# Performance work log

Hardware: AMD Instinct MI355X
Metric: run time of the kernel (lower is better)

## Reference

```python
import jax, jax.numpy as jnp
import numpy as np

B, C, H, W, K = 4, 64, 128, 128, 3
K2 = K * K
PAD = (K - 1) // 2  # same padding for 3x3


def setup_inputs() -> dict:
    key = jax.random.key(0)
    ks = jax.random.split(key, 9)
    s = 0.05
    return {
        "x": jax.random.normal(ks[0], (B, C, H, W), jnp.float32),
        "inter": jax.random.normal(ks[1], (B, C, H, W), jnp.float32),
        # offset/mask predictor conv: input cat([x, inter]) -> 3*K2 channels (dy, dx, mask)
        "w_offset": jax.random.normal(ks[2], (3 * K2, 2 * C, K, K), jnp.float32) * s,
        "b_offset": jnp.zeros((3 * K2,), jnp.float32),
        # deformable conv weight (bias=False per DGM init)
        "w_dcn": jax.random.normal(ks[3], (C, C, K, K), jnp.float32) * s,
        # SFT gamma branch: two 1x1 convs (bias=False)
        "w_g1": jax.random.normal(ks[4], (C, C), jnp.float32) * s,
        "w_g2": jax.random.normal(ks[5], (C, C), jnp.float32) * s,
        # SFT beta branch: two 1x1 convs (bias=False)
        "w_b1": jax.random.normal(ks[6], (C, C), jnp.float32) * s,
        "w_b2": jax.random.normal(ks[7], (C, C), jnp.float32) * s,
    }


def _lrelu(v):
    # LeakyReLU(0.1)
    return jnp.where(v >= 0, v, 0.1 * v)


def _conv(x, w, b=None):
    y = jax.lax.conv_general_dilated(
        x, w, window_strides=(1, 1), padding=[(PAD, PAD), (PAD, PAD)],
        dimension_numbers=("NCHW", "OIHW", "NCHW"))
    if b is not None:
        y = y + b[None, :, None, None]
    return y


def _bilinear_gather(x, py, px):
    """x: [B,C,H,W]; py, px: [B,K2,H,W] float sample coords.
    Returns samples [B,K2,H,W,C]; out-of-bounds treated as zero (DCN zero-pad)."""
    y0 = jnp.floor(py)
    x0 = jnp.floor(px)
    wy = (py - y0)[..., None]
    wx = (px - x0)[..., None]

    def gather(yi, xi):
        valid = ((yi >= 0) & (yi < H) & (xi >= 0) & (xi < W)).astype(x.dtype)
        yc = jnp.clip(yi, 0, H - 1).astype(jnp.int32)
        xc = jnp.clip(xi, 0, W - 1).astype(jnp.int32)
        bidx = jnp.arange(B)[:, None, None, None]
        v = x[bidx, :, yc, xc]  # advanced indexing -> [B,K2,H,W,C]
        return v * valid[..., None]

    v00 = gather(y0, x0)
    v01 = gather(y0, x0 + 1)
    v10 = gather(y0 + 1, x0)
    v11 = gather(y0 + 1, x0 + 1)
    return (v00 * (1 - wy) * (1 - wx) + v01 * (1 - wy) * wx
            + v10 * wy * (1 - wx) + v11 * wy * wx)


def _dgm_forward(x, inter, w_offset, b_offset, w_dcn, w_g1, w_g2, w_b1, w_b2):
    # --- WADCN branch: modulated deformable conv, offsets predicted from cat(x, inter)
    om = _conv(jnp.concatenate([x, inter], axis=1), w_offset, b_offset)  # [B,3K2,H,W]
    dy, dx, m = jnp.split(om, 3, axis=1)  # each [B,K2,H,W]
    mask = jax.nn.sigmoid(m)

    ky, kx = jnp.meshgrid(jnp.arange(K), jnp.arange(K), indexing="ij")
    ky = ky.reshape(K2).astype(x.dtype)
    kx = kx.reshape(K2).astype(x.dtype)
    hh = jnp.arange(H, dtype=x.dtype)
    ww = jnp.arange(W, dtype=x.dtype)
    # sample coords: base grid + kernel-tap offset + learned offset
    py = hh[None, None, :, None] + (ky - PAD)[None, :, None, None] + dy  # [B,K2,H,W]
    px = ww[None, None, None, :] + (kx - PAD)[None, :, None, None] + dx

    samp = _bilinear_gather(x, py, px) * mask[..., None]  # [B,K2,H,W,C]
    dcn_out = jnp.einsum("bkhwc,ock->bohw", samp, w_dcn.reshape(C, C, K2))

    # --- SFT branch: two 1x1-conv + LeakyReLU chains producing gamma/beta
    gamma = jnp.einsum("oc,bchw->bohw", w_g2,
                       _lrelu(jnp.einsum("oc,bchw->bohw", w_g1, inter)))
    beta = jnp.einsum("oc,bchw->bohw", w_b2,
                      _lrelu(jnp.einsum("oc,bchw->bohw", w_b1, inter)))
    sft_out = x * gamma + beta

    # --- fused residual combine (DGM.relu is defined but never applied)
    return x + dcn_out + sft_out


def reference(x, inter, w_offset, b_offset, w_dcn, w_g1, w_g2, w_b1, w_b2):
    return _dgm_forward(x, inter, w_offset, b_offset, w_dcn, w_g1, w_g2, w_b1, w_b2)
```

## Files before the change

kernel.cpp:

```cpp
#include <hip/hip_runtime.h>
#include <hip/hip_bf16.h>
#include <math.h>

#define BB 4
#define CC 64
#define HH 128
#define WW 128
#define HW (HH*WW)
#define NPIX (BB*HW)

typedef __attribute__((ext_vector_type(8))) short short8;
typedef __attribute__((ext_vector_type(4))) float f32x4;

__device__ __forceinline__ float bf2f(ushort u) {
  union { unsigned u; float f; } v; v.u = ((unsigned)u) << 16; return v.f;
}
__device__ __forceinline__ ushort f2bf(float f) {
  __hip_bfloat16 h = __float2bfloat16(f); return *(ushort*)&h;
}

__global__ __launch_bounds__(256) void k_prep(
    const float* __restrict__ x, const float* __restrict__ inter,
    const float* __restrict__ w_off, const float* __restrict__ w_dcn,
    const float* __restrict__ wg1, const float* __restrict__ wb1,
    const float* __restrict__ wg2, const float* __restrict__ wb2,
    ushort* __restrict__ x_clh, ushort* __restrict__ inter_clh,
    ushort* __restrict__ wfb, ushort* __restrict__ wdT,
    ushort* __restrict__ w1gb, ushort* __restrict__ w1bb,
    ushort* __restrict__ w2gb, ushort* __restrict__ w2bb,
    float* __restrict__ zp) {
  __shared__ __align__(16) float tile[64 * 128];
  int blk = blockIdx.x;
  int tid = threadIdx.x;
  if (blk < 1024) {
    int sel = blk >> 9;
    int bh = blk & 511;
    int b = bh >> 7, h = bh & 127;
    const float* src = sel ? inter : x;
    ushort* dst = sel ? inter_clh : x_clh;
    const float* sp = src + (size_t)(b * 64) * HW + h * WW;
#pragma unroll
    for (int it = 0; it < 8; ++it) {
      int idx = it * 256 + tid;
      int c = idx >> 5, wq = idx & 31;
      float4 v = *(const float4*)(sp + (size_t)c * HW + wq * 4);
      int s = (c >> 3) & 7;
      *(float4*)(&tile[c * 128 + ((wq ^ s) << 2)]) = v;
    }
    __syncthreads();
    ushort* dp = dst + ((size_t)b * HW + h * WW) * 64;
#pragma unroll
    for (int it = 0; it < 4; ++it) {
      int idx = it * 256 + tid;
      int w = idx >> 3, c8 = idx & 7;
      short8 outv;
#pragma unroll
      for (int j = 0; j < 8; ++j) {
        int c = c8 * 8 + j;
        int sl = (w >> 2) ^ c8;
        float f = tile[c * 128 + (sl << 2) + (w & 3)];
        outv[j] = (short)f2bf(f);
      }
      *(short8*)(dp + (size_t)w * 64 + c8 * 8) = outv;
    }
  } else if (blk < 1168) {
    int i = (blk - 1024) * 256 + tid;
    if (i < 64) zp[i] = 0.f;
    if (i < 9 * 32 * 128) {
      int tap = i >> 12, rem = i & 4095, m = rem >> 7, c = rem & 127;
      float v = (m < 27) ? w_off[(size_t)(m * 128 + c) * 9 + tap] : 0.f;
      wfb[i] = f2bf(v);
    }
  } else if (blk < 1312) {
    int i = (blk - 1168) * 256 + tid;
    if (i < 64 * 64 * 9) {
      int o = i / 576, rem = i % 576, k = rem >> 6, c = rem & 63;
      wdT[i] = f2bf(w_dcn[(o * 64 + c) * 9 + k]);
    }
  } else {
    int i = (blk - 1312) * 256 + tid;
    int m = i >> 12, j = i & 4095;
    const float* src = (m == 0) ? wg1 : (m == 1) ? wb1 : (m == 2) ? wg2 : wb2;
    ushort* dst = (m == 0) ? w1gb : (m == 1) ? w1bb : (m == 2) ? w2gb : w2bb;
    dst[j] = f2bf(src[j]);
  }
}

#define CPITCH 72
#define SPITCH 200
#define NPX 32
#define FPX 72

__global__ __launch_bounds__(256) void k_omega(
    const float* __restrict__ x, const ushort* __restrict__ x_clh,
    const ushort* __restrict__ inter_clh,
    const float* __restrict__ b_off, const ushort* __restrict__ wfb,
    const ushort* __restrict__ wdT,
    const ushort* __restrict__ w1gb, const ushort* __restrict__ w1bb,
    const ushort* __restrict__ w2gb, const ushort* __restrict__ w2bb,
    const ushort* __restrict__ zp16, float* __restrict__ out) {
  __shared__ __align__(16) ushort BIGB[6 * 34 * CPITCH];
  ushort* S  = BIGB;
  ushort* Sg = BIGB + 6400;
  ushort* Sb = Sg + NPX * FPX;
  int*   cy  = (int*)(BIGB + 6400);
  int*   cx  = cy + 288;
  float* cwy = (float*)(cx + 288);
  float* cwx = cwy + 288;
  float* cm  = cwx + 288;
  float* oml = (float*)(BIGB + 11008);

  int tid = threadIdx.x;
  int wave = tid >> 6, lane = tid & 63;
  int quad = lane >> 4, col = lane & 15;
  int rr = lane >> 3, g = lane & 7;
  int bid = blockIdx.x;
  int wid = (bid & 7) * 256 + (bid >> 3);
  int pg0 = wid * NPX;
  int b = pg0 >> 14, hw0 = pg0 & 16383;
  int h = hw0 >> 7, w0 = hw0 & 127;
  int pt = wave >> 1, mt = wave & 1;
  int o_base = __builtin_amdgcn_readfirstlane(wave * 16);

  {
    int ch = (tid & 7) * 8;
    unsigned bbase = (unsigned)b * HW;
#pragma unroll
    for (int it = 0; it < 7; ++it) {
      int e = it * 32 + (tid >> 3);
      if (e < 204) {
        int srcrow = e / 34, pxl = e % 34;
        int src = srcrow / 3, row = srcrow % 3;
        int hs = h + row - 1;
        int ps = w0 + pxl - 1;
        bool ok = ((unsigned)hs < 128u) && ((unsigned)ps < 128u);
        int hc = hs < 0 ? 0 : (hs > 127 ? 127 : hs);
        int pc = ps < 0 ? 0 : (ps > 127 ? 127 : ps);
        const ushort* sb = src ? inter_clh : x_clh;
        short8 v = *(const short8*)(sb + ((size_t)(bbase + (hc << 7) + pc)) * 64 + ch);
        short8 z = {0, 0, 0, 0, 0, 0, 0, 0};
        if (!ok) v = z;
        *(short8*)(&BIGB[e * CPITCH + ch]) = v;
      }
    }
  }
  __syncthreads();

  f32x4 accx = {0.f, 0.f, 0.f, 0.f}, acci = {0.f, 0.f, 0.f, 0.f};
  {
    const ushort* wb0 = wfb + (size_t)(mt * 16 + col) * 128 + quad * 8;
    int pxb = pt * 16 + col;
#pragma unroll
    for (int ky = 0; ky < 3; ++ky) {
#pragma unroll
      for (int kx = 0; kx < 3; ++kx) {
        int tap = ky * 3 + kx;
        const ushort* wt = wb0 + (size_t)tap * 4096;
#pragma unroll
        for (int ks = 0; ks < 2; ++ks) {
          short8 a0 = *(const short8*)(wt + ks * 32);
          short8 b0 = *(const short8*)(&BIGB[(ky * 34 + pxb + kx) * CPITCH + ks * 32 + quad * 8]);
          accx = __builtin_amdgcn_mfma_f32_16x16x32_bf16(a0, b0, accx, 0, 0, 0);
          short8 a1 = *(const short8*)(wt + 64 + ks * 32);
          short8 b1 = *(const short8*)(&BIGB[((3 + ky) * 34 + pxb + kx) * CPITCH + ks * 32 + quad * 8]);
          acci = __builtin_amdgcn_mfma_f32_16x16x32_bf16(a1, b1, acci, 0, 0, 0);
        }
      }
    }
  }
  __syncthreads();

#pragma unroll
  for (int r = 0; r < 4; ++r) {
    int o = mt * 16 + quad * 4 + r;
    if (o < 27) oml[o * 33 + pt * 16 + col] = accx[r] + acci[r];
  }

  f32x4 ag[2], ab[2];
#pragma unroll
  for (int nt = 0; nt < 2; ++nt) {
    ag[nt] = (f32x4){0.f, 0.f, 0.f, 0.f};
    ab[nt] = (f32x4){0.f, 0.f, 0.f, 0.f};
  }
#pragma unroll
  for (int ks = 0; ks < 2; ++ks) {
    short8 a_g = *(const short8*)(w1gb + (size_t)(o_base + col) * 64 + ks * 32 + quad * 8);
    short8 a_b = *(const short8*)(w1bb + (size_t)(o_base + col) * 64 + ks * 32 + quad * 8);
#pragma unroll
    for (int nt = 0; nt < 2; ++nt) {
      short8 bf = *(const short8*)(inter_clh + (size_t)(pg0 + nt * 16 + col) * 64 + ks * 32 + quad * 8);
      ag[nt] = __builtin_amdgcn_mfma_f32_16x16x32_bf16(a_g, bf, ag[nt], 0, 0, 0);
      ab[nt] = __builtin_amdgcn_mfma_f32_16x16x32_bf16(a_b, bf, ab[nt], 0, 0, 0);
    }
  }
#pragma unroll
  for (int nt = 0; nt < 2; ++nt) {
    int px = nt * 16 + col;
    ushort pkg[4], pkb[4];
#pragma unroll
    for (int r = 0; r < 4; ++r) {
      float vg = ag[nt][r]; vg = vg >= 0.f ? vg : 0.1f * vg;
      float vb = ab[nt][r]; vb = vb >= 0.f ? vb : 0.1f * vb;
      pkg[r] = f2bf(vg); pkb[r] = f2bf(vb);
    }
    *(uint2*)(&Sg[px * FPX + o_base + quad * 4]) = *(uint2*)pkg;
    *(uint2*)(&Sb[px * FPX + o_base + quad * 4]) = *(uint2*)pkb;
  }
  __syncthreads();

  f32x4 gg[2], gb[2];
#pragma unroll
  for (int nt = 0; nt < 2; ++nt) {
    gg[nt] = (f32x4){0.f, 0.f, 0.f, 0.f};
    gb[nt] = (f32x4){0.f, 0.f, 0.f, 0.f};
  }
#pragma unroll
  for (int ks = 0; ks < 2; ++ks) {
    short8 a_g = *(const short8*)(w2gb + (size_t)(o_base + col) * 64 + ks * 32 + quad * 8);
    short8 a_b = *(const short8*)(w2bb + (size_t)(o_base + col) * 64 + ks * 32 + quad * 8);
#pragma unroll
    for (int nt = 0; nt < 2; ++nt) {
      short8 bgf = *(const short8*)(Sg + (nt * 16 + col) * FPX + ks * 32 + quad * 8);
      short8 bbf = *(const short8*)(Sb + (nt * 16 + col) * FPX + ks * 32 + quad * 8);
      gg[nt] = __builtin_amdgcn_mfma_f32_16x16x32_bf16(a_g, bgf, gg[nt], 0, 0, 0);
      gb[nt] = __builtin_amdgcn_mfma_f32_16x16x32_bf16(a_b, bbf, gb[nt], 0, 0, 0);
    }
  }
  float xv[2][4];
#pragma unroll
  for (int nt = 0; nt < 2; ++nt)
#pragma unroll
    for (int r = 0; r < 4; ++r) {
      int o = o_base + quad * 4 + r;
      xv[nt][r] = x[(size_t)(b * 64 + o) * HW + hw0 + nt * 16 + col];
    }
  __syncthreads();

  for (int i = tid; i < 9 * NPX; i += 256) {
    int k = i >> 5, p = i & 31;
    float dy = oml[k * 33 + p] + b_off[k];
    float dx = oml[(9 + k) * 33 + p] + b_off[9 + k];
    float mz = oml[(18 + k) * 33 + p] + b_off[18 + k];
    float py = (float)(h + (k / 3) - 1) + dy;
    float px = (float)(w0 + p + (k % 3) - 1) + dx;
    float y0f = floorf(py), x0f = floorf(px);
    cy[i] = (int)y0f;
    cx[i] = (int)x0f;
    cwy[i] = py - y0f;
    cwx[i] = px - x0f;
    cm[i] = 1.f / (1.f + __expf(-mz));
  }

  f32x4 acc[2];
  acc[0] = (f32x4){0.f, 0.f, 0.f, 0.f};
  acc[1] = (f32x4){0.f, 0.f, 0.f, 0.f};

  const ushort* bp = x_clh + (size_t)b * HW * 64;

  for (int chunk = 0; chunk < 3; ++chunk) {
    __syncthreads();
#pragma unroll
    for (int it = 0; it < 3; ++it) {
      int p = wave * 8 + rr;
      int idx = (chunk * 3 + it) * NPX + p;
      int y0 = cy[idx], x0 = cx[idx];
      float wy = cwy[idx], wx = cwx[idx], m = cm[idx];
      bool yok0 = (unsigned)y0 < 128u, yok1 = (unsigned)(y0 + 1) < 128u;
      bool xok0 = (unsigned)x0 < 128u, xok1 = (unsigned)(x0 + 1) < 128u;
      const ushort* r0 = bp + ((size_t)(int)((y0 << 7) + x0)) * 64 + g * 8;
      const ushort* r1 = r0 + (size_t)WW * 64;
      short8 s00 = *(const short8*)((yok0 && xok0) ? r0 : zp16);
      short8 s01 = *(const short8*)((yok0 && xok1) ? (r0 + 64) : zp16);
      short8 s10 = *(const short8*)((yok1 && xok0) ? r1 : zp16);
      short8 s11 = *(const short8*)((yok1 && xok1) ? (r1 + 64) : zp16);
      short8 outv;
#pragma unroll
      for (int j = 0; j < 8; ++j) {
        float v00 = bf2f((ushort)s00[j]), v01 = bf2f((ushort)s01[j]);
        float v10 = bf2f((ushort)s10[j]), v11 = bf2f((ushort)s11[j]);
        float top = v00 + (v01 - v00) * wx;
        float bot = v10 + (v11 - v10) * wx;
        float val = top + (bot - top) * wy;
        outv[j] = (short)f2bf(val * m);
      }
      *(short8*)(&S[p * SPITCH + it * 64 + g * 8]) = outv;
    }
    __syncthreads();
    const ushort* wrow = wdT + (size_t)(o_base + col) * 576 + chunk * 192 + quad * 8;
    const ushort* srow = S + quad * 8;
#pragma unroll
    for (int ks = 0; ks < 6; ++ks) {
      short8 a = *(const short8*)(wrow + ks * 32);
#pragma unroll
      for (int nt = 0; nt < 2; ++nt) {
        short8 bf = *(const short8*)(srow + (nt * 16 + col) * SPITCH + ks * 32);
        acc[nt] = __builtin_amdgcn_mfma_f32_16x16x32_bf16(a, bf, acc[nt], 0, 0, 0);
      }
    }
  }

#pragma unroll
  for (int nt = 0; nt < 2; ++nt) {
#pragma unroll
    for (int r = 0; r < 4; ++r) {
      int o = o_base + quad * 4 + r;
      size_t idx = (size_t)(b * 64 + o) * HW + hw0 + nt * 16 + col;
      out[idx] = xv[nt][r] + xv[nt][r] * gg[nt][r] + gb[nt][r] + acc[nt][r];
    }
  }
}

extern "C" void kernel_launch(void* const* d_in, const int* in_sizes, int n_in,
                              void* d_out, int out_size, void* d_ws, size_t ws_size,
                              hipStream_t stream) {
  const float* x     = (const float*)d_in[0];
  const float* inter = (const float*)d_in[1];
  const float* w_off = (const float*)d_in[2];
  const float* b_off = (const float*)d_in[3];
  const float* w_dcn = (const float*)d_in[4];
  const float* wg1   = (const float*)d_in[5];
  const float* wg2   = (const float*)d_in[6];
  const float* wb1   = (const float*)d_in[7];
  const float* wb2   = (const float*)d_in[8];
  float* out = (float*)d_out;

  float* ws        = (float*)d_ws;
  ushort* x_clh    = (ushort*)ws;
  ushort* inter_clh= (ushort*)(ws + 2097152);
  ushort* wfb      = (ushort*)(ws + 4194304);
  ushort* wdT      = (ushort*)(ws + 4212736);
  ushort* w1gb     = (ushort*)(ws + 4231168);
  ushort* w1bb     = (ushort*)(ws + 4233216);
  ushort* w2gb     = (ushort*)(ws + 4235264);
  ushort* w2bb     = (ushort*)(ws + 4237312);
  float* zp        = ws + 4239360;

  k_prep<<<1376, 256, 0, stream>>>(x, inter, w_off, w_dcn, wg1, wb1, wg2, wb2,
                                   x_clh, inter_clh, wfb, wdT,
                                   w1gb, w1bb, w2gb, w2bb, zp);

  k_omega<<<2048, 256, 0, stream>>>(x, x_clh, inter_clh, b_off, wfb, wdT,
                                    w1gb, w1bb, w2gb, w2bb,
                                    (const ushort*)zp, out);
}
```

Before: 169.2 us.

## Feed bilinear samples directly into MFMA registers, dropping LDS staging in DCN

The wave-to-output mapping changes so each wave owns 16 pixels and 32 output channels. Each lane now gathers and interpolates its own pixel's channels in the exact B-operand layout of the MFMA. This removes the shared-memory sample buffer, the per-chunk barriers and the LDS round trip. The SFT epilogue is also partly folded into a single value early, which frees registers. In exchange, each sampled pixel is gathered by two waves (one per output-channel half), doubling global gather traffic. The weight A-fragments are also loaded per tap from global memory.

```diff
diff --git a/kernel.cpp b/kernel.cpp
--- a/kernel.cpp
+++ b/kernel.cpp
@@ -87,7 +87,6 @@
 }
 
 #define CPITCH 72
-#define SPITCH 200
 #define NPX 32
 #define FPX 72
 
@@ -100,7 +99,6 @@
     const ushort* __restrict__ w2gb, const ushort* __restrict__ w2bb,
     const ushort* __restrict__ zp16, float* __restrict__ out) {
   __shared__ __align__(16) ushort BIGB[6 * 34 * CPITCH];
-  ushort* S  = BIGB;
   ushort* Sg = BIGB + 6400;
   ushort* Sb = Sg + NPX * FPX;
   int*   cy  = (int*)(BIGB + 6400);
@@ -113,14 +111,14 @@
   int tid = threadIdx.x;
   int wave = tid >> 6, lane = tid & 63;
   int quad = lane >> 4, col = lane & 15;
-  int rr = lane >> 3, g = lane & 7;
   int bid = blockIdx.x;
   int wid = (bid & 7) * 256 + (bid >> 3);
   int pg0 = wid * NPX;
   int b = pg0 >> 14, hw0 = pg0 & 16383;
   int h = hw0 >> 7, w0 = hw0 & 127;
   int pt = wave >> 1, mt = wave & 1;
-  int o_base = __builtin_amdgcn_readfirstlane(wave * 16);
+  int ob = __builtin_amdgcn_readfirstlane(mt * 32);
+  int mypx = pt * 16 + col;
 
   {
     int ch = (tid & 7) * 8;
@@ -178,61 +176,61 @@
 
   f32x4 ag[2], ab[2];
 #pragma unroll
-  for (int nt = 0; nt < 2; ++nt) {
-    ag[nt] = (f32x4){0.f, 0.f, 0.f, 0.f};
-    ab[nt] = (f32x4){0.f, 0.f, 0.f, 0.f};
+  for (int og = 0; og < 2; ++og) {
+    ag[og] = (f32x4){0.f, 0.f, 0.f, 0.f};
+    ab[og] = (f32x4){0.f, 0.f, 0.f, 0.f};
   }
 #pragma unroll
   for (int ks = 0; ks < 2; ++ks) {
-    short8 a_g = *(const short8*)(w1gb + (size_t)(o_base + col) * 64 + ks * 32 + quad * 8);
-    short8 a_b = *(const short8*)(w1bb + (size_t)(o_base + col) * 64 + ks * 32 + quad * 8);
-#pragma unroll
-    for (int nt = 0; nt < 2; ++nt) {
-      short8 bf = *(const short8*)(inter_clh + (size_t)(pg0 + nt * 16 + col) * 64 + ks * 32 + quad * 8);
-      ag[nt] = __builtin_amdgcn_mfma_f32_16x16x32_bf16(a_g, bf, ag[nt], 0, 0, 0);
-      ab[nt] = __builtin_amdgcn_mfma_f32_16x16x32_bf16(a_b, bf, ab[nt], 0, 0, 0);
-    }
-  }
-#pragma unroll
-  for (int nt = 0; nt < 2; ++nt) {
-    int px = nt * 16 + col;
+    short8 bf = *(const short8*)(inter_clh + (size_t)(pg0 + mypx) * 64 + ks * 32 + quad * 8);
+#pragma unroll
+    for (int og = 0; og < 2; ++og) {
+      short8 a_g = *(const short8*)(w1gb + (size_t)(ob + og * 16 + col) * 64 + ks * 32 + quad * 8);
+      short8 a_b = *(const short8*)(w1bb + (size_t)(ob + og * 16 + col) * 64 + ks * 32 + quad * 8);
+      ag[og] = __builtin_amdgcn_mfma_f32_16x16x32_bf16(a_g, bf, ag[og], 0, 0, 0);
+      ab[og] = __builtin_amdgcn_mfma_f32_16x16x32_bf16(a_b, bf, ab[og], 0, 0, 0);
+    }
+  }
+#pragma unroll
+  for (int og = 0; og < 2; ++og) {
     ushort pkg[4], pkb[4];
 #pragma unroll
     for (int r = 0; r < 4; ++r) {
-      float vg = ag[nt][r]; vg = vg >= 0.f ? vg : 0.1f * vg;
-      float vb = ab[nt][r]; vb = vb >= 0.f ? vb : 0.1f * vb;
+      float vg = ag[og][r]; vg = vg >= 0.f ? vg : 0.1f * vg;
+      float vb = ab[og][r]; vb = vb >= 0.f ? vb : 0.1f * vb;
       pkg[r] = f2bf(vg); pkb[r] = f2bf(vb);
     }
-    *(uint2*)(&Sg[px * FPX + o_base + quad * 4]) = *(uint2*)pkg;
-    *(uint2*)(&Sb[px * FPX + o_base + quad * 4]) = *(uint2*)pkb;
+    *(uint2*)(&Sg[mypx * FPX + ob + og * 16 + quad * 4]) = *(uint2*)pkg;
+    *(uint2*)(&Sb[mypx * FPX + ob + og * 16 + quad * 4]) = *(uint2*)pkb;
   }
   __syncthreads();
 
   f32x4 gg[2], gb[2];
 #pragma unroll
-  for (int nt = 0; nt < 2; ++nt) {
-    gg[nt] = (f32x4){0.f, 0.f, 0.f, 0.f};
-    gb[nt] = (f32x4){0.f, 0.f, 0.f, 0.f};
+  for (int og = 0; og < 2; ++og) {
+    gg[og] = (f32x4){0.f, 0.f, 0.f, 0.f};
+    gb[og] = (f32x4){0.f, 0.f, 0.f, 0.f};
   }
 #pragma unroll
   for (int ks = 0; ks < 2; ++ks) {
-    short8 a_g = *(const short8*)(w2gb + (size_t)(o_base + col) * 64 + ks * 32 + quad * 8);
-    short8 a_b = *(const short8*)(w2bb + (size_t)(o_base + col) * 64 + ks * 32 + quad * 8);
-#pragma unroll
-    for (int nt = 0; nt < 2; ++nt) {
-      short8 bgf = *(const short8*)(Sg + (nt * 16 + col) * FPX + ks * 32 + quad * 8);
-      short8 bbf = *(const short8*)(Sb + (nt * 16 + col) * FPX + ks * 32 + quad * 8);
-      gg[nt] = __builtin_amdgcn_mfma_f32_16x16x32_bf16(a_g, bgf, gg[nt], 0, 0, 0);
-      gb[nt] = __builtin_amdgcn_mfma_f32_16x16x32_bf16(a_b, bbf, gb[nt], 0, 0, 0);
-    }
-  }
-  float xv[2][4];
-#pragma unroll
-  for (int nt = 0; nt < 2; ++nt)
+    short8 bgf = *(const short8*)(Sg + mypx * FPX + ks * 32 + quad * 8);
+    short8 bbf = *(const short8*)(Sb + mypx * FPX + ks * 32 + quad * 8);
+#pragma unroll
+    for (int og = 0; og < 2; ++og) {
+      short8 a_g = *(const short8*)(w2gb + (size_t)(ob + og * 16 + col) * 64 + ks * 32 + quad * 8);
+      short8 a_b = *(const short8*)(w2bb + (size_t)(ob + og * 16 + col) * 64 + ks * 32 + quad * 8);
+      gg[og] = __builtin_amdgcn_mfma_f32_16x16x32_bf16(a_g, bgf, gg[og], 0, 0, 0);
+      gb[og] = __builtin_amdgcn_mfma_f32_16x16x32_bf16(a_b, bbf, gb[og], 0, 0, 0);
+    }
+  }
+  float ev[2][4];
+#pragma unroll
+  for (int og = 0; og < 2; ++og)
 #pragma unroll
     for (int r = 0; r < 4; ++r) {
-      int o = o_base + quad * 4 + r;
-      xv[nt][r] = x[(size_t)(b * 64 + o) * HW + hw0 + nt * 16 + col];
+      int o = ob + og * 16 + quad * 4 + r;
+      float xv = x[(size_t)(b * 64 + o) * HW + hw0 + mypx];
+      ev[og][r] = xv + xv * gg[og][r] + gb[og][r];
     }
   __syncthreads();
 
@@ -250,30 +248,38 @@
     cwx[i] = px - x0f;
     cm[i] = 1.f / (1.f + __expf(-mz));
   }
+  __syncthreads();
 
   f32x4 acc[2];
   acc[0] = (f32x4){0.f, 0.f, 0.f, 0.f};
   acc[1] = (f32x4){0.f, 0.f, 0.f, 0.f};
 
-  const ushort* bp = x_clh + (size_t)b * HW * 64;
-
-  for (int chunk = 0; chunk < 3; ++chunk) {
-    __syncthreads();
-#pragma unroll
-    for (int it = 0; it < 3; ++it) {
-      int p = wave * 8 + rr;
-      int idx = (chunk * 3 + it) * NPX + p;
-      int y0 = cy[idx], x0 = cx[idx];
-      float wy = cwy[idx], wx = cwx[idx], m = cm[idx];
-      bool yok0 = (unsigned)y0 < 128u, yok1 = (unsigned)(y0 + 1) < 128u;
-      bool xok0 = (unsigned)x0 < 128u, xok1 = (unsigned)(x0 + 1) < 128u;
-      const ushort* r0 = bp + ((size_t)(int)((y0 << 7) + x0)) * 64 + g * 8;
-      const ushort* r1 = r0 + (size_t)WW * 64;
-      short8 s00 = *(const short8*)((yok0 && xok0) ? r0 : zp16);
-      short8 s01 = *(const short8*)((yok0 && xok1) ? (r0 + 64) : zp16);
-      short8 s10 = *(const short8*)((yok1 && xok0) ? r1 : zp16);
-      short8 s11 = *(const short8*)((yok1 && xok1) ? (r1 + 64) : zp16);
-      short8 outv;
+  const ushort* bp  = x_clh + (size_t)b * HW * 64 + quad * 8;
+  const ushort* zpq = zp16 + quad * 8;
+  const ushort* wd0 = wdT + (size_t)(ob + col) * 576 + quad * 8;
+  const ushort* wd1 = wd0 + (size_t)16 * 576;
+
+#pragma unroll 3
+  for (int t = 0; t < 9; ++t) {
+    int idx = t * NPX + mypx;
+    int y0 = cy[idx], x0 = cx[idx];
+    float wy = cwy[idx], wx = cwx[idx], m = cm[idx];
+    bool yok0 = (unsigned)y0 < 128u, yok1 = (unsigned)(y0 + 1) < 128u;
+    bool xok0 = (unsigned)x0 < 128u, xok1 = (unsigned)(x0 + 1) < 128u;
+    const ushort* r0 = bp + (long long)(int)((y0 << 7) + x0) * 64;
+    const ushort* r1 = r0 + (size_t)WW * 64;
+    const ushort* p00 = (yok0 && xok0) ? r0 : zpq;
+    const ushort* p01 = (yok0 && xok1) ? (r0 + 64) : zpq;
+    const ushort* p10 = (yok1 && xok0) ? r1 : zpq;
+    const ushort* p11 = (yok1 && xok1) ? (r1 + 64) : zpq;
+#pragma unroll
+    for (int kk = 0; kk < 2; ++kk) {
+      int off = kk * 32;
+      short8 s00 = *(const short8*)(p00 + off);
+      short8 s01 = *(const short8*)(p01 + off);
+      short8 s10 = *(const short8*)(p10 + off);
+      short8 s11 = *(const short8*)(p11 + off);
+      short8 bfr;
 #pragma unroll
       for (int j = 0; j < 8; ++j) {
         float v00 = bf2f((ushort)s00[j]), v01 = bf2f((ushort)s01[j]);
@@ -281,33 +287,23 @@
         float top = v00 + (v01 - v00) * wx;
         float bot = v10 + (v11 - v10) * wx;
         float val = top + (bot - top) * wy;
-        outv[j] = (short)f2bf(val * m);
+        bfr[j] = (short)f2bf(val * m);
       }
-      *(short8*)(&S[p * SPITCH + it * 64 + g * 8]) = outv;
-    }
-    __syncthreads();
-    const ushort* wrow = wdT + (size_t)(o_base + col) * 576 + chunk * 192 + quad * 8;
-    const ushort* srow = S + quad * 8;
-#pragma unroll
-    for (int ks = 0; ks < 6; ++ks) {
-      short8 a = *(const short8*)(wrow + ks * 32);
-#pragma unroll
-      for (int nt = 0; nt < 2; ++nt) {
-        short8 bf = *(const short8*)(srow + (nt * 16 + col) * SPITCH + ks * 32);
-        acc[nt] = __builtin_amdgcn_mfma_f32_16x16x32_bf16(a, bf, acc[nt], 0, 0, 0);
-      }
-    }
-  }
-
-#pragma unroll
-  for (int nt = 0; nt < 2; ++nt) {
+      short8 a0 = *(const short8*)(wd0 + t * 64 + off);
+      short8 a1 = *(const short8*)(wd1 + t * 64 + off);
+      acc[0] = __builtin_amdgcn_mfma_f32_16x16x32_bf16(a0, bfr, acc[0], 0, 0, 0);
+      acc[1] = __builtin_amdgcn_mfma_f32_16x16x32_bf16(a1, bfr, acc[1], 0, 0, 0);
+    }
+  }
+
+#pragma unroll
+  for (int og = 0; og < 2; ++og)
 #pragma unroll
     for (int r = 0; r < 4; ++r) {
-      int o = o_base + quad * 4 + r;
-      size_t idx = (size_t)(b * 64 + o) * HW + hw0 + nt * 16 + col;
-      out[idx] = xv[nt][r] + xv[nt][r] * gg[nt][r] + gb[nt][r] + acc[nt][r];
-    }
-  }
+      int o = ob + og * 16 + quad * 4 + r;
+      size_t idx = (size_t)(b * 64 + o) * HW + hw0 + mypx;
+      out[idx] = ev[og][r] + acc[og][r];
+    }
 }
 
 extern "C" void kernel_launch(void* const* d_in, const int* in_sizes, int n_in,
```

Measured after the change: 240.3 us. +42.0%, slower.

## Split offset-conv halo staging into two passes to shrink LDS footprint

Applied to the files above, without the earlier changes.

The offset/mask conv previously staged both x and inter halo tiles (6 rows × 34 px) into shared memory at once. It now stages one source at a time into a single 3-row halo buffer, runs its MFMA accumulation, then reuses the buffer for the other source. The shared-memory regions are re-laid-out so the total LDS allocation shrinks, aiming for higher occupancy. The cost is an extra pair of barriers and serialized load/compute between the two passes, with less overlap of global loads.

```diff
diff --git a/kernel.cpp b/kernel.cpp
--- a/kernel.cpp
+++ b/kernel.cpp
@@ -99,16 +99,17 @@
     const ushort* __restrict__ w1gb, const ushort* __restrict__ w1bb,
     const ushort* __restrict__ w2gb, const ushort* __restrict__ w2bb,
     const ushort* __restrict__ zp16, float* __restrict__ out) {
-  __shared__ __align__(16) ushort BIGB[6 * 34 * CPITCH];
-  ushort* S  = BIGB;
-  ushort* Sg = BIGB + 6400;
-  ushort* Sb = Sg + NPX * FPX;
-  int*   cy  = (int*)(BIGB + 6400);
+  __shared__ __align__(16) ushort LDSB[9280];
+  ushort* halo = LDSB;
+  ushort* Sg = LDSB;
+  ushort* Sb = LDSB + 2304;
+  float* oml = (float*)(LDSB + 4608);
+  int*   cy  = (int*)LDSB;
   int*   cx  = cy + 288;
   float* cwy = (float*)(cx + 288);
   float* cwx = cwy + 288;
   float* cm  = cwx + 288;
-  float* oml = (float*)(BIGB + 11008);
+  ushort* S  = LDSB + 2880;
 
   int tid = threadIdx.x;
   int wave = tid >> 6, lane = tid & 63;
@@ -122,53 +123,52 @@
   int pt = wave >> 1, mt = wave & 1;
   int o_base = __builtin_amdgcn_readfirstlane(wave * 16);
 
+  f32x4 accx = {0.f, 0.f, 0.f, 0.f}, acci = {0.f, 0.f, 0.f, 0.f};
   {
     int ch = (tid & 7) * 8;
     unsigned bbase = (unsigned)b * HW;
-#pragma unroll
-    for (int it = 0; it < 7; ++it) {
-      int e = it * 32 + (tid >> 3);
-      if (e < 204) {
-        int srcrow = e / 34, pxl = e % 34;
-        int src = srcrow / 3, row = srcrow % 3;
-        int hs = h + row - 1;
-        int ps = w0 + pxl - 1;
-        bool ok = ((unsigned)hs < 128u) && ((unsigned)ps < 128u);
-        int hc = hs < 0 ? 0 : (hs > 127 ? 127 : hs);
-        int pc = ps < 0 ? 0 : (ps > 127 ? 127 : ps);
-        const ushort* sb = src ? inter_clh : x_clh;
-        short8 v = *(const short8*)(sb + ((size_t)(bbase + (hc << 7) + pc)) * 64 + ch);
-        short8 z = {0, 0, 0, 0, 0, 0, 0, 0};
-        if (!ok) v = z;
-        *(short8*)(&BIGB[e * CPITCH + ch]) = v;
-      }
-    }
-  }
-  __syncthreads();
-
-  f32x4 accx = {0.f, 0.f, 0.f, 0.f}, acci = {0.f, 0.f, 0.f, 0.f};
-  {
     const ushort* wb0 = wfb + (size_t)(mt * 16 + col) * 128 + quad * 8;
     int pxb = pt * 16 + col;
-#pragma unroll
-    for (int ky = 0; ky < 3; ++ky) {
-#pragma unroll
-      for (int kx = 0; kx < 3; ++kx) {
-        int tap = ky * 3 + kx;
-        const ushort* wt = wb0 + (size_t)tap * 4096;
-#pragma unroll
-        for (int ks = 0; ks < 2; ++ks) {
-          short8 a0 = *(const short8*)(wt + ks * 32);
-          short8 b0 = *(const short8*)(&BIGB[(ky * 34 + pxb + kx) * CPITCH + ks * 32 + quad * 8]);
-          accx = __builtin_amdgcn_mfma_f32_16x16x32_bf16(a0, b0, accx, 0, 0, 0);
-          short8 a1 = *(const short8*)(wt + 64 + ks * 32);
-          short8 b1 = *(const short8*)(&BIGB[((3 + ky) * 34 + pxb + kx) * CPITCH + ks * 32 + quad * 8]);
-          acci = __builtin_amdgcn_mfma_f32_16x16x32_bf16(a1, b1, acci, 0, 0, 0);
+#pragma unroll 1
+    for (int pass = 0; pass < 2; ++pass) {
+      const ushort* sb = pass ? inter_clh : x_clh;
+#pragma unroll
+      for (int it = 0; it < 4; ++it) {
+        int e = it * 32 + (tid >> 3);
+        if (e < 102) {
+          int row = e / 34, pxl = e % 34;
+          int hs = h + row - 1;
+          int ps = w0 + pxl - 1;
+          bool ok = ((unsigned)hs < 128u) && ((unsigned)ps < 128u);
+          int hc = hs < 0 ? 0 : (hs > 127 ? 127 : hs);
+          int pc = ps < 0 ? 0 : (ps > 127 ? 127 : ps);
+          short8 v = *(const short8*)(sb + ((size_t)(bbase + (hc << 7) + pc)) * 64 + ch);
+          short8 z = {0, 0, 0, 0, 0, 0, 0, 0};
+          if (!ok) v = z;
+          *(short8*)(&halo[e * CPITCH + ch]) = v;
         }
       }
-    }
-  }
-  __syncthreads();
+      __syncthreads();
+      int aoff = pass ? 64 : 0;
+      f32x4 accp = {0.f, 0.f, 0.f, 0.f};
+#pragma unroll
+      for (int ky = 0; ky < 3; ++ky) {
+#pragma unroll
+        for (int kx = 0; kx < 3; ++kx) {
+          int tap = ky * 3 + kx;
+          const ushort* wt = wb0 + (size_t)tap * 4096 + aoff;
+#pragma unroll
+          for (int ks = 0; ks < 2; ++ks) {
+            short8 a0 = *(const short8*)(wt + ks * 32);
+            short8 b0 = *(const short8*)(&halo[(ky * 34 + pxb + kx) * CPITCH + ks * 32 + quad * 8]);
+            accp = __builtin_amdgcn_mfma_f32_16x16x32_bf16(a0, b0, accp, 0, 0, 0);
+          }
+        }
+      }
+      if (pass) acci = accp; else accx = accp;
+      __syncthreads();
+    }
+  }
 
 #pragma unroll
   for (int r = 0; r < 4; ++r) {
```

Measured after the change: 172.3 us. About the same (+1.8%).
